# Performance work log

Hardware: AMD Instinct MI355X
Metric: run time of the kernel (lower is better)

The kernel has to match this reference:

```python
import jax, jax.numpy as jnp
import numpy as np

# dims
B, T, HORIZON, N = 32, 12, 12, 512
IN, OUT, H, P = 1, 1, 64, 32
S, ML, MG, DE = 12, 64, 32, 10  # S_local == S_global


def setup_inputs() -> dict:
    key = jax.random.key(0)
    ks = jax.random.split(key, 12)
    f = lambda k, shp: jax.random.normal(k, shp, dtype=jnp.float32)
    return {
        "source": f(ks[0], (B, T, N, IN)),
        "local_mem": f(ks[1], (ML, S, P)) * 0.1,
        "global_mem": f(ks[2], (MG, S, P)) * 0.1,
        "Wq": f(ks[3], (H, P)) / np.sqrt(H),
        "bq": jnp.zeros((P,), jnp.float32),
        "node_emb": f(ks[4], (N, DE)) * 0.1,
        "weight_pool": f(ks[5], (DE, 2 * P, H)) / np.sqrt(2 * P),
        "Wz": f(ks[6], (IN + H, H)) / np.sqrt(IN + H), "bz": jnp.zeros((H,), jnp.float32),
        "Wr": f(ks[7], (IN + H, H)) / np.sqrt(IN + H), "br": jnp.zeros((H,), jnp.float32),
        "Wc": f(ks[8], (IN + H, H)) / np.sqrt(IN + H), "bc": jnp.zeros((H,), jnp.float32),
        "Wo": f(ks[9], (H, OUT)) / np.sqrt(H), "bo": jnp.zeros((OUT,), jnp.float32),
    }


def _forward(source, local_mem, global_mem, Wq, bq, node_emb, weight_pool,
             Wz, bz, Wr, br, Wc, bc, Wo, bo):
    b, t, n, _ = source.shape
    hdim = Wz.shape[1]
    s = local_mem.shape[1]
    # node-specific hypernetwork weights: [N, 2P, H]
    nsw = jnp.einsum('nd,dfh->nfh', node_emb, weight_pool)
    lmean = local_mem.mean(axis=1)   # [ML, P]
    gmean = global_mem.mean(axis=1)  # [MG, P]

    def dcn(buffer):  # buffer: [B, N, S, H]
        q = jnp.einsum('bnsh,hp->bnsp', buffer, Wq) + bq          # [B,N,S,P]
        a_l = jax.nn.softmax(jnp.einsum('bnsp,msp->bnm', q, local_mem), axis=-1)
        a_g = jax.nn.softmax(jnp.einsum('bnsp,msp->bnm', q, global_mem), axis=-1)
        # context mean over S == attn @ mean-over-S memory
        lc = a_l @ lmean                                           # [B,N,P]
        gc = a_g @ gmean                                           # [B,N,P]
        fused = jnp.concatenate([lc, gc], axis=-1)                 # [B,N,2P]
        return jnp.einsum('bnf,nfh->bnh', fused, nsw)              # [B,N,H]

    def cell(x_t, h_prev, buffer):
        ctx = dcn(buffer)
        comb = jnp.concatenate([x_t, h_prev], axis=-1)
        z = jax.nn.sigmoid(comb @ Wz + bz)
        r = jax.nn.sigmoid(comb @ Wr + br)
        comb2 = jnp.concatenate([x_t, r * h_prev], axis=-1)
        hc = jnp.tanh(comb2 @ Wc + bc + ctx)
        return (1.0 - z) * h_prev + z * hc

    h0 = jnp.zeros((b, n, hdim), source.dtype)
    buf0 = jnp.zeros((b, n, s, hdim), source.dtype)

    def enc_step(carry, x_t):
        h, buf = carry
        h = cell(x_t, h, buf)
        buf = jax.lax.stop_gradient(
            jnp.concatenate([buf[:, :, 1:], h[:, :, None]], axis=2))
        return (h, buf), None

    (h, buf), _ = jax.lax.scan(enc_step, (h0, buf0), jnp.moveaxis(source, 1, 0))

    def dec_step(carry, _):
        h, buf, x = carry
        h = cell(x, h, buf)
        buf = jax.lax.stop_gradient(
            jnp.concatenate([buf[:, :, 1:], h[:, :, None]], axis=2))
        y = h @ Wo + bo
        return (h, buf, y), y

    _, ys = jax.lax.scan(dec_step, (h, buf, source[:, -1]), None, length=HORIZON)
    return jnp.moveaxis(ys, 0, 1)  # [B, horizon, N, OUT]


def reference(source, local_mem, global_mem, Wq, bq, node_emb, weight_pool,
              Wz, bz, Wr, br, Wc, bc, Wo, bo):
    return _forward(source, local_mem, global_mem, Wq, bq, node_emb, weight_pool,
                    Wz, bz, Wr, br, Wc, bc, Wo, bo)
```

## Files before the change

### kernel.cpp

```cpp
#include <hip/hip_runtime.h>


typedef short short8 __attribute__((ext_vector_type(8)));
typedef float f32x4 __attribute__((ext_vector_type(4)));

#define DEV static __device__ __forceinline__

DEV unsigned short f2bf(float f) {
  union { float f; unsigned u; } v; v.f = f;
  unsigned r = v.u + 0x7FFFu + ((v.u >> 16) & 1u);
  return (unsigned short)(r >> 16);
}
DEV float bf2f(unsigned short b) {
  union { unsigned u; float f; } v; v.u = ((unsigned)b) << 16;
  return v.f;
}
DEV unsigned cvtpk(float a, float b) {
  unsigned r;
  asm("v_cvt_pk_bf16_f32 %0, %1, %2" : "=v"(r) : "v"(a), "v"(b));
  return r;
}
DEV float rcpf(float x) { return __builtin_amdgcn_rcpf(x); }

#define WG_OFF  36864
#define WQ_OFF  61440
#define LM_OFF  63488
#define GM_OFF  65536
#define WS_TOT  66560

#define L_W     0
#define L_WQ    49152
#define L_LM    53248
#define L_SCR   59392
#define SCR_STRIDE 21504
#define SMEM_BYTES 145408

#define R_AL 0
#define R_AG 2048
#define R_FU 3072
#define R_HH 5120
#define R_HL 7168
#define R_RH 9216
#define R_RL 11264
#define R_NSW 13312
#define R_QQ 0

#define MFMA16(a, b, c) __builtin_amdgcn_mfma_f32_16x16x32_bf16((a), (b), (c), 0, 0, 0)

DEV int scat_off(int col, int g) {
  int kp = col & 31;
  return ((col >> 5) << 10) + ((kp >> 3) << 8) + (g << 6) + ((kp & 7) << 1);
}
DEV void scat4(char* p, f32x4 v) {
  unsigned p0 = cvtpk(v[0], v[1]), p1 = cvtpk(v[2], v[3]);
  *(unsigned short*)(p)      = (unsigned short)p0;
  *(unsigned short*)(p + 16) = (unsigned short)(p0 >> 16);
  *(unsigned short*)(p + 32) = (unsigned short)p1;
  *(unsigned short*)(p + 48) = (unsigned short)(p1 >> 16);
}
DEV void scat4_hilo(char* ph, char* pl, f32x4 v) {
  unsigned p0 = cvtpk(v[0], v[1]), p1 = cvtpk(v[2], v[3]);
  float h0 = __uint_as_float(p0 << 16), h1 = __uint_as_float(p0 & 0xFFFF0000u);
  float h2 = __uint_as_float(p1 << 16), h3 = __uint_as_float(p1 & 0xFFFF0000u);
  unsigned q0 = cvtpk(v[0] - h0, v[1] - h1), q1 = cvtpk(v[2] - h2, v[3] - h3);
  *(unsigned short*)(ph)      = (unsigned short)p0;
  *(unsigned short*)(ph + 16) = (unsigned short)(p0 >> 16);
  *(unsigned short*)(ph + 32) = (unsigned short)p1;
  *(unsigned short*)(ph + 48) = (unsigned short)(p1 >> 16);
  *(unsigned short*)(pl)      = (unsigned short)q0;
  *(unsigned short*)(pl + 16) = (unsigned short)(q0 >> 16);
  *(unsigned short*)(pl + 32) = (unsigned short)q1;
  *(unsigned short*)(pl + 48) = (unsigned short)(q1 >> 16);
}

__global__ __launch_bounds__(256, 1) void dyna_prep(
    const float* __restrict__ lmem, const float* __restrict__ gmem,
    const float* __restrict__ Wq, const float* __restrict__ Wz,
    const float* __restrict__ Wr, const float* __restrict__ Wc,
    unsigned short* __restrict__ ws)
{
  int i = blockIdx.x * 256 + threadIdx.x;
  if (i >= WS_TOT) return;

  if (i < WG_OFF) {
    int f = i >> 9, r = i & 511, lane = r >> 3, j = r & 7;
    int g = lane >> 4, u = lane & 15;
    int s = f / 6, nt = f % 6;
    int m = nt * 16 + u, p = g * 8 + j;
    float v = (m < 64) ? lmem[(m * 12 + s) * 32 + p]
                       : gmem[((m - 64) * 12 + s) * 32 + p];
    ws[i] = f2bf(v);
  } else if (i < WQ_OFF) {
    int t = i - WG_OFF;
    int f = t >> 9, r = t & 511, lane = r >> 3, j = r & 7;
    int g = lane >> 4, u = lane & 15;
    int hl = f & 1, kc = (f >> 1) & 1, nt = (f >> 2) & 3, gate = f >> 4;
    int k = kc * 32 + g * 8 + j, col = nt * 16 + u;
    const float* W = (gate == 0) ? Wz : (gate == 1) ? Wr : Wc;
    float w = W[(1 + k) * 64 + col];
    if (hl) { float hi = bf2f(f2bf(w)); ws[i] = f2bf(w - hi); }
    else ws[i] = f2bf(w);
  } else if (i < LM_OFF) {
    int t = i - WQ_OFF;
    int f = t >> 9, r = t & 511, lane = r >> 3, j = r & 7;
    int g = lane >> 4, u = lane & 15;
    int kc = f & 1, nt = f >> 1;
    int k = kc * 32 + g * 8 + j, col = nt * 16 + u;
    ws[i] = f2bf(Wq[k * 32 + col]);
  } else if (i < GM_OFF) {
    int t = i - LM_OFF;
    int f = t >> 9, r = t & 511, lane = r >> 3, j = r & 7;
    int g = lane >> 4, u = lane & 15;
    int kc = f >> 1, nt = f & 1;
    int k = kc * 32 + g * 8 + j, p = nt * 16 + u;
    float s = 0.f;
    for (int ss = 0; ss < 12; ++ss) s += lmem[(k * 12 + ss) * 32 + p];
    ws[i] = f2bf(s * (1.0f / 12.0f));
  } else {
    int t = i - GM_OFF;
    int f = t >> 9, r = t & 511, lane = r >> 3, j = r & 7;
    int g = lane >> 4, u = lane & 15;
    int nt = f;
    int k = g * 8 + j, p = nt * 16 + u;
    float s = 0.f;
    for (int ss = 0; ss < 12; ++ss) s += gmem[(k * 12 + ss) * 32 + p];
    ws[i] = f2bf(s * (1.0f / 12.0f));
  }
}

__global__ __launch_bounds__(256, 1) void dyna_main(
    const float* __restrict__ src, const float* __restrict__ emb,
    const float* __restrict__ pool, const float* __restrict__ bq,
    const float* __restrict__ Wz, const float* __restrict__ bz,
    const float* __restrict__ Wr, const float* __restrict__ br,
    const float* __restrict__ Wc, const float* __restrict__ bc,
    const float* __restrict__ Wo, const float* __restrict__ bo,
    const unsigned short* __restrict__ ws, float* __restrict__ out)
{
  extern __shared__ char smem[];
  const int tid = threadIdx.x;
  const int lane = tid & 63, wid = tid >> 6;
  const int g = lane >> 4, u = lane & 15;
  const int n = blockIdx.x * 2 + (wid >> 1);
  const int hb = wid & 1;

  {
    const short8* s8 = (const short8*)ws;
    short8* d8 = (short8*)smem;
    for (int i = tid; i < 3712; i += 256) d8[i] = s8[4608 + i];
  }

  short8 marr[72];
  #pragma unroll
  for (int f = 0; f < 72; ++f)
    marr[f] = *(const short8*)(ws + (f << 9) + lane * 8);

  char* SCR = smem + L_SCR + wid * SCR_STRIDE;

  #pragma unroll
  for (int kc = 0; kc < 2; ++kc)
    #pragma unroll
    for (int nt = 0; nt < 4; ++nt) {
      short8 v;
      #pragma unroll
      for (int j = 0; j < 8; ++j) {
        int k = kc * 32 + g * 8 + j, col = nt * 16 + u;
        float s = 0.f;
        #pragma unroll
        for (int d = 0; d < 10; ++d)
          s += emb[n * 10 + d] * pool[(d * 64 + k) * 64 + col];
        v[j] = (short)f2bf(s);
      }
      *(short8*)(SCR + R_NSW + ((kc * 4 + nt) << 10) + (lane << 4)) = v;
    }

  float w0z[4], w0r[4], w0c[4], bzv[4], brv[4], bcv[4], wov[4], bqv[2];
  #pragma unroll
  for (int nt = 0; nt < 4; ++nt) {
    int col = nt * 16 + u;
    w0z[nt] = Wz[col]; w0r[nt] = Wr[col]; w0c[nt] = Wc[col];
    bzv[nt] = bz[col]; brv[nt] = br[col]; bcv[nt] = bc[col];
    wov[nt] = Wo[col];
  }
  bqv[0] = bq[u]; bqv[1] = bq[16 + u];
  const float bov = bo[0];

  short8 qh[12];
  {
    short8 qi;
    #pragma unroll
    for (int j = 0; j < 8; ++j) qi[j] = (short)f2bf(bq[g * 8 + j]);
    #pragma unroll
    for (int s = 0; s < 12; ++s) qh[s] = qi;
  }
  f32x4 hreg[4];
  #pragma unroll
  for (int nt = 0; nt < 4; ++nt) hreg[nt] = (f32x4){0.f, 0.f, 0.f, 0.f};
  float xreg[4] = {0.f, 0.f, 0.f, 0.f};

  #pragma unroll
  for (int nt = 0; nt < 4; ++nt) {
    int so = scat_off(nt * 16 + u, g);
    scat4_hilo(SCR + R_HH + so, SCR + R_HL + so, hreg[nt]);
  }

  __syncthreads();

  for (int t = 0; t < 24; ++t) {
    if (t <= 12) {
      int tt = t < 12 ? t : 11;
      #pragma unroll
      for (int reg = 0; reg < 4; ++reg) {
        int b = hb * 16 + g * 4 + reg;
        xreg[reg] = src[(b * 12 + tt) * 512 + n];
      }
    }

    short8 hhi0 = *(const short8*)(SCR + R_HH + (lane << 4));
    short8 hhi1 = *(const short8*)(SCR + R_HH + 1024 + (lane << 4));
    short8 hlo0 = *(const short8*)(SCR + R_HL + (lane << 4));
    short8 hlo1 = *(const short8*)(SCR + R_HL + 1024 + (lane << 4));

    f32x4 sacc[6];
    #pragma unroll
    for (int nt = 0; nt < 6; ++nt) sacc[nt] = (f32x4){0.f, 0.f, 0.f, 0.f};
    __builtin_amdgcn_s_setprio(1);
    #pragma unroll
    for (int s = 0; s < 12; ++s) {
      #pragma unroll
      for (int nt = 0; nt < 6; ++nt)
        sacc[nt] = MFMA16(qh[s], marr[s * 6 + nt], sacc[nt]);
    }
    __builtin_amdgcn_s_setprio(0);

    #pragma unroll
    for (int nt = 0; nt < 6; ++nt)
      #pragma unroll
      for (int reg = 0; reg < 4; ++reg)
        sacc[nt][reg] = __expf(sacc[nt][reg]);
    float invl[4], invg[4];
    #pragma unroll
    for (int reg = 0; reg < 4; ++reg) {
      float sl = (sacc[0][reg] + sacc[1][reg]) + (sacc[2][reg] + sacc[3][reg]);
      sl += __shfl_xor(sl, 1); sl += __shfl_xor(sl, 2);
      sl += __shfl_xor(sl, 4); sl += __shfl_xor(sl, 8);
      invl[reg] = rcpf(sl);
      float sg = sacc[4][reg] + sacc[5][reg];
      sg += __shfl_xor(sg, 1); sg += __shfl_xor(sg, 2);
      sg += __shfl_xor(sg, 4); sg += __shfl_xor(sg, 8);
      invg[reg] = rcpf(sg);
    }

    #pragma unroll
    for (int nt = 0; nt < 4; ++nt)
      scat4(SCR + R_AL + scat_off(nt * 16 + u, g), sacc[nt]);
    #pragma unroll
    for (int nt = 0; nt < 2; ++nt)
      scat4(SCR + R_AG + scat_off(nt * 16 + u, g), sacc[4 + nt]);

    f32x4 zacc[4], racc[4];
    #pragma unroll
    for (int nt = 0; nt < 4; ++nt) {
      zacc[nt] = (f32x4){0.f, 0.f, 0.f, 0.f};
      racc[nt] = (f32x4){0.f, 0.f, 0.f, 0.f};
    }
    #pragma unroll
    for (int kc = 0; kc < 2; ++kc) {
      short8 hh = kc ? hhi1 : hhi0;
      short8 hl = kc ? hlo1 : hlo0;
      #pragma unroll
      for (int nt = 0; nt < 4; ++nt) {
        short8 wzh = *(const short8*)(smem + L_W + ((((0 + nt) * 2 + kc) * 2 + 0) << 10) + (lane << 4));
        short8 wzl = *(const short8*)(smem + L_W + ((((0 + nt) * 2 + kc) * 2 + 1) << 10) + (lane << 4));
        zacc[nt] = MFMA16(hh, wzh, zacc[nt]);
        zacc[nt] = MFMA16(hl, wzh, zacc[nt]);
        zacc[nt] = MFMA16(hh, wzl, zacc[nt]);
        short8 wrh = *(const short8*)(smem + L_W + ((((4 + nt) * 2 + kc) * 2 + 0) << 10) + (lane << 4));
        short8 wrl = *(const short8*)(smem + L_W + ((((4 + nt) * 2 + kc) * 2 + 1) << 10) + (lane << 4));
        racc[nt] = MFMA16(hh, wrh, racc[nt]);
        racc[nt] = MFMA16(hl, wrh, racc[nt]);
        racc[nt] = MFMA16(hh, wrl, racc[nt]);
      }
    }

    #pragma unroll
    for (int nt = 0; nt < 4; ++nt)
      #pragma unroll
      for (int reg = 0; reg < 4; ++reg) {
        float zv = zacc[nt][reg] + xreg[reg] * w0z[nt] + bzv[nt];
        zacc[nt][reg] = rcpf(1.0f + __expf(-zv));
        float rv = racc[nt][reg] + xreg[reg] * w0r[nt] + brv[nt];
        racc[nt][reg] = rcpf(1.0f + __expf(-rv));
      }

    #pragma unroll
    for (int nt = 0; nt < 4; ++nt) {
      int so = scat_off(nt * 16 + u, g);
      f32x4 rh;
      #pragma unroll
      for (int reg = 0; reg < 4; ++reg) rh[reg] = racc[nt][reg] * hreg[nt][reg];
      scat4_hilo(SCR + R_RH + so, SCR + R_RL + so, rh);
    }

    short8 alf0 = *(const short8*)(SCR + R_AL + (lane << 4));
    short8 alf1 = *(const short8*)(SCR + R_AL + 1024 + (lane << 4));
    short8 agf  = *(const short8*)(SCR + R_AG + (lane << 4));
    f32x4 lacc[2], gacc[2];
    #pragma unroll
    for (int nt = 0; nt < 2; ++nt) {
      lacc[nt] = (f32x4){0.f, 0.f, 0.f, 0.f};
      gacc[nt] = (f32x4){0.f, 0.f, 0.f, 0.f};
      short8 lm0 = *(const short8*)(smem + L_LM + ((0 * 2 + nt) << 10) + (lane << 4));
      short8 lm1 = *(const short8*)(smem + L_LM + ((1 * 2 + nt) << 10) + (lane << 4));
      short8 gm  = *(const short8*)(smem + L_LM + 4096 + (nt << 10) + (lane << 4));
      lacc[nt] = MFMA16(alf0, lm0, lacc[nt]);
      lacc[nt] = MFMA16(alf1, lm1, lacc[nt]);
      gacc[nt] = MFMA16(agf, gm, gacc[nt]);
    }

    short8 rhh0 = *(const short8*)(SCR + R_RH + (lane << 4));
    short8 rhh1 = *(const short8*)(SCR + R_RH + 1024 + (lane << 4));
    short8 rhl0 = *(const short8*)(SCR + R_RL + (lane << 4));
    short8 rhl1 = *(const short8*)(SCR + R_RL + 1024 + (lane << 4));
    f32x4 hacc[4];
    #pragma unroll
    for (int nt = 0; nt < 4; ++nt) hacc[nt] = (f32x4){0.f, 0.f, 0.f, 0.f};
    #pragma unroll
    for (int kc = 0; kc < 2; ++kc) {
      short8 hh = kc ? rhh1 : rhh0;
      short8 hl = kc ? rhl1 : rhl0;
      #pragma unroll
      for (int nt = 0; nt < 4; ++nt) {
        short8 wch = *(const short8*)(smem + L_W + ((((8 + nt) * 2 + kc) * 2 + 0) << 10) + (lane << 4));
        short8 wcl = *(const short8*)(smem + L_W + ((((8 + nt) * 2 + kc) * 2 + 1) << 10) + (lane << 4));
        hacc[nt] = MFMA16(hh, wch, hacc[nt]);
        hacc[nt] = MFMA16(hl, wch, hacc[nt]);
        hacc[nt] = MFMA16(hh, wcl, hacc[nt]);
      }
    }

    #pragma unroll
    for (int nt = 0; nt < 2; ++nt) {
      f32x4 lv, gv;
      #pragma unroll
      for (int reg = 0; reg < 4; ++reg) {
        lv[reg] = lacc[nt][reg] * invl[reg];
        gv[reg] = gacc[nt][reg] * invg[reg];
      }
      scat4(SCR + R_FU + scat_off(nt * 16 + u, g), lv);
      scat4(SCR + R_FU + scat_off(32 + nt * 16 + u, g), gv);
    }
    short8 fuf0 = *(const short8*)(SCR + R_FU + (lane << 4));
    short8 fuf1 = *(const short8*)(SCR + R_FU + 1024 + (lane << 4));

    f32x4 cacc[4];
    #pragma unroll
    for (int nt = 0; nt < 4; ++nt) {
      short8 nf0 = *(const short8*)(SCR + R_NSW + ((0 * 4 + nt) << 10) + (lane << 4));
      short8 nf1 = *(const short8*)(SCR + R_NSW + ((1 * 4 + nt) << 10) + (lane << 4));
      cacc[nt] = (f32x4){0.f, 0.f, 0.f, 0.f};
      cacc[nt] = MFMA16(fuf0, nf0, cacc[nt]);
      cacc[nt] = MFMA16(fuf1, nf1, cacc[nt]);
    }

    #pragma unroll
    for (int nt = 0; nt < 4; ++nt)
      #pragma unroll
      for (int reg = 0; reg < 4; ++reg) {
        float pv = hacc[nt][reg] + cacc[nt][reg] + xreg[reg] * w0c[nt] + bcv[nt];
        float tdenom = rcpf(1.0f + __expf(2.0f * pv));
        float hc = 1.0f - 2.0f * tdenom;
        float zv = zacc[nt][reg];
        hreg[nt][reg] = (1.0f - zv) * hreg[nt][reg] + zv * hc;
      }

    #pragma unroll
    for (int nt = 0; nt < 4; ++nt) {
      int so = scat_off(nt * 16 + u, g);
      scat4_hilo(SCR + R_HH + so, SCR + R_HL + so, hreg[nt]);
    }
    short8 nh0 = *(const short8*)(SCR + R_HH + (lane << 4));
    short8 nh1 = *(const short8*)(SCR + R_HH + 1024 + (lane << 4));

    f32x4 qacc[2];
    #pragma unroll
    for (int nt = 0; nt < 2; ++nt) {
      short8 wq0 = *(const short8*)(smem + L_WQ + ((nt * 2 + 0) << 10) + (lane << 4));
      short8 wq1 = *(const short8*)(smem + L_WQ + ((nt * 2 + 1) << 10) + (lane << 4));
      qacc[nt] = (f32x4){0.f, 0.f, 0.f, 0.f};
      qacc[nt] = MFMA16(nh0, wq0, qacc[nt]);
      qacc[nt] = MFMA16(nh1, wq1, qacc[nt]);
      #pragma unroll
      for (int reg = 0; reg < 4; ++reg) qacc[nt][reg] += bqv[nt];
    }
    #pragma unroll
    for (int nt = 0; nt < 2; ++nt)
      scat4(SCR + R_QQ + scat_off(nt * 16 + u, g), qacc[nt]);
    short8 qnf = *(const short8*)(SCR + R_QQ + (lane << 4));
    #pragma unroll
    for (int s = 0; s < 11; ++s) qh[s] = qh[s + 1];
    qh[11] = qnf;

    if (t >= 12) {
      #pragma unroll
      for (int reg = 0; reg < 4; ++reg) {
        float yp = hreg[0][reg] * wov[0] + hreg[1][reg] * wov[1] +
                   hreg[2][reg] * wov[2] + hreg[3][reg] * wov[3];
        yp += __shfl_xor(yp, 1); yp += __shfl_xor(yp, 2);
        yp += __shfl_xor(yp, 4); yp += __shfl_xor(yp, 8);
        float yv = yp + bov;
        xreg[reg] = yv;
        if (u == 0) {
          int b = hb * 16 + g * 4 + reg;
          out[(b * 12 + (t - 12)) * 512 + n] = yv;
        }
      }
    }
  }
}

extern "C" void kernel_launch(void* const* d_in, const int* in_sizes, int n_in,
                              void* d_out, int out_size, void* d_ws, size_t ws_size,
                              hipStream_t stream) {
  const float* src  = (const float*)d_in[0];
  const float* lmem = (const float*)d_in[1];
  const float* gmem = (const float*)d_in[2];
  const float* Wq   = (const float*)d_in[3];
  const float* bq   = (const float*)d_in[4];
  const float* emb  = (const float*)d_in[5];
  const float* pool = (const float*)d_in[6];
  const float* Wz   = (const float*)d_in[7];
  const float* bz   = (const float*)d_in[8];
  const float* Wr   = (const float*)d_in[9];
  const float* br   = (const float*)d_in[10];
  const float* Wc   = (const float*)d_in[11];
  const float* bc   = (const float*)d_in[12];
  const float* Wo   = (const float*)d_in[13];
  const float* bo   = (const float*)d_in[14];
  float* out = (float*)d_out;
  unsigned short* ws = (unsigned short*)d_ws;

  dyna_prep<<<260, 256, 0, stream>>>(lmem, gmem, Wq, Wz, Wr, Wc, ws);

  (void)hipFuncSetAttribute((const void*)dyna_main,
                            hipFuncAttributeMaxDynamicSharedMemorySize,
                            SMEM_BYTES);
  dyna_main<<<256, 256, SMEM_BYTES, stream>>>(src, emb, pool, bq, Wz, bz, Wr, br,
                                              Wc, bc, Wo, bo, ws, out);
}
```

Measured before the change: 211.9 us.

## Precompute next-step attention scores and offload row reductions to MFMA

The attention-score MFMA chain is restructured so that the 11 of 12 query-history terms still valid after the history shift are accumulated mid-step for the next timestep. This leaves only one MFMA per tile on the critical path at the start of each step, and the rest can overlap with the gate GEMMs. Softmax denominators now come from MFMA against an all-ones bf16 matrix instead of cross-lane shuffles. The decoder output projection uses split-bf16 MFMA in place of a shuffle reduction. The costs are extra live accumulator registers, and denominators built from bf16-rounded exponentials.

```diff
diff --git a/kernel.cpp b/kernel.cpp
--- a/kernel.cpp
+++ b/kernel.cpp
@@ -143,6 +143,7 @@
   const int g = lane >> 4, u = lane & 15;
   const int n = blockIdx.x * 2 + (wid >> 1);
   const int hb = wid & 1;
+  const f32x4 ZERO4 = {0.f, 0.f, 0.f, 0.f};
 
   {
     const short8* s8 = (const short8*)ws;
@@ -174,13 +175,25 @@
       *(short8*)(SCR + R_NSW + ((kc * 4 + nt) << 10) + (lane << 4)) = v;
     }
 
-  float w0z[4], w0r[4], w0c[4], bzv[4], brv[4], bcv[4], wov[4], bqv[2];
+  short8 ones, woh[2], wol[2];
+  #pragma unroll
+  for (int j = 0; j < 8; ++j) ones[j] = (short)0x3F80;
+  #pragma unroll
+  for (int kc = 0; kc < 2; ++kc)
+    #pragma unroll
+    for (int j = 0; j < 8; ++j) {
+      float w = Wo[kc * 32 + g * 8 + j];
+      unsigned short hi = f2bf(w);
+      woh[kc][j] = (short)hi;
+      wol[kc][j] = (short)f2bf(w - bf2f(hi));
+    }
+
+  float w0z[4], w0r[4], w0c[4], bzv[4], brv[4], bcv[4], bqv[2];
   #pragma unroll
   for (int nt = 0; nt < 4; ++nt) {
     int col = nt * 16 + u;
     w0z[nt] = Wz[col]; w0r[nt] = Wr[col]; w0c[nt] = Wc[col];
     bzv[nt] = bz[col]; brv[nt] = br[col]; bcv[nt] = bc[col];
-    wov[nt] = Wo[col];
   }
   bqv[0] = bq[u]; bqv[1] = bq[16 + u];
   const float bov = bo[0];
@@ -195,8 +208,17 @@
   }
   f32x4 hreg[4];
   #pragma unroll
-  for (int nt = 0; nt < 4; ++nt) hreg[nt] = (f32x4){0.f, 0.f, 0.f, 0.f};
+  for (int nt = 0; nt < 4; ++nt) hreg[nt] = ZERO4;
   float xreg[4] = {0.f, 0.f, 0.f, 0.f};
+
+  f32x4 sacc_next[6];
+  #pragma unroll
+  for (int nt = 0; nt < 6; ++nt) sacc_next[nt] = ZERO4;
+  #pragma unroll
+  for (int s = 0; s <= 10; ++s)
+    #pragma unroll
+    for (int nt = 0; nt < 6; ++nt)
+      sacc_next[nt] = MFMA16(qh[s], marr[s * 6 + nt], sacc_next[nt]);
 
   #pragma unroll
   for (int nt = 0; nt < 4; ++nt) {
@@ -223,34 +245,14 @@
 
     f32x4 sacc[6];
     #pragma unroll
-    for (int nt = 0; nt < 6; ++nt) sacc[nt] = (f32x4){0.f, 0.f, 0.f, 0.f};
-    __builtin_amdgcn_s_setprio(1);
-    #pragma unroll
-    for (int s = 0; s < 12; ++s) {
-      #pragma unroll
-      for (int nt = 0; nt < 6; ++nt)
-        sacc[nt] = MFMA16(qh[s], marr[s * 6 + nt], sacc[nt]);
-    }
-    __builtin_amdgcn_s_setprio(0);
+    for (int nt = 0; nt < 6; ++nt)
+      sacc[nt] = MFMA16(qh[11], marr[66 + nt], sacc_next[nt]);
 
     #pragma unroll
     for (int nt = 0; nt < 6; ++nt)
       #pragma unroll
       for (int reg = 0; reg < 4; ++reg)
         sacc[nt][reg] = __expf(sacc[nt][reg]);
-    float invl[4], invg[4];
-    #pragma unroll
-    for (int reg = 0; reg < 4; ++reg) {
-      float sl = (sacc[0][reg] + sacc[1][reg]) + (sacc[2][reg] + sacc[3][reg]);
-      sl += __shfl_xor(sl, 1); sl += __shfl_xor(sl, 2);
-      sl += __shfl_xor(sl, 4); sl += __shfl_xor(sl, 8);
-      invl[reg] = rcpf(sl);
-      float sg = sacc[4][reg] + sacc[5][reg];
-      sg += __shfl_xor(sg, 1); sg += __shfl_xor(sg, 2);
-      sg += __shfl_xor(sg, 4); sg += __shfl_xor(sg, 8);
-      invg[reg] = rcpf(sg);
-    }
-
     #pragma unroll
     for (int nt = 0; nt < 4; ++nt)
       scat4(SCR + R_AL + scat_off(nt * 16 + u, g), sacc[nt]);
@@ -258,11 +260,19 @@
     for (int nt = 0; nt < 2; ++nt)
       scat4(SCR + R_AG + scat_off(nt * 16 + u, g), sacc[4 + nt]);
 
+    #pragma unroll
+    for (int nt = 0; nt < 6; ++nt) sacc_next[nt] = ZERO4;
+    #pragma unroll
+    for (int s = 1; s <= 11; ++s)
+      #pragma unroll
+      for (int nt = 0; nt < 6; ++nt)
+        sacc_next[nt] = MFMA16(qh[s], marr[(s - 1) * 6 + nt], sacc_next[nt]);
+
     f32x4 zacc[4], racc[4];
     #pragma unroll
     for (int nt = 0; nt < 4; ++nt) {
-      zacc[nt] = (f32x4){0.f, 0.f, 0.f, 0.f};
-      racc[nt] = (f32x4){0.f, 0.f, 0.f, 0.f};
+      zacc[nt] = ZERO4;
+      racc[nt] = ZERO4;
     }
     #pragma unroll
     for (int kc = 0; kc < 2; ++kc) {
@@ -305,11 +315,16 @@
     short8 alf0 = *(const short8*)(SCR + R_AL + (lane << 4));
     short8 alf1 = *(const short8*)(SCR + R_AL + 1024 + (lane << 4));
     short8 agf  = *(const short8*)(SCR + R_AG + (lane << 4));
+    f32x4 lsum = ZERO4;
+    lsum = MFMA16(alf0, ones, lsum);
+    lsum = MFMA16(alf1, ones, lsum);
+    f32x4 gsum = ZERO4;
+    gsum = MFMA16(agf, ones, gsum);
     f32x4 lacc[2], gacc[2];
     #pragma unroll
     for (int nt = 0; nt < 2; ++nt) {
-      lacc[nt] = (f32x4){0.f, 0.f, 0.f, 0.f};
-      gacc[nt] = (f32x4){0.f, 0.f, 0.f, 0.f};
+      lacc[nt] = ZERO4;
+      gacc[nt] = ZERO4;
       short8 lm0 = *(const short8*)(smem + L_LM + ((0 * 2 + nt) << 10) + (lane << 4));
       short8 lm1 = *(const short8*)(smem + L_LM + ((1 * 2 + nt) << 10) + (lane << 4));
       short8 gm  = *(const short8*)(smem + L_LM + 4096 + (nt << 10) + (lane << 4));
@@ -324,7 +339,7 @@
     short8 rhl1 = *(const short8*)(SCR + R_RL + 1024 + (lane << 4));
     f32x4 hacc[4];
     #pragma unroll
-    for (int nt = 0; nt < 4; ++nt) hacc[nt] = (f32x4){0.f, 0.f, 0.f, 0.f};
+    for (int nt = 0; nt < 4; ++nt) hacc[nt] = ZERO4;
     #pragma unroll
     for (int kc = 0; kc < 2; ++kc) {
       short8 hh = kc ? rhh1 : rhh0;
@@ -339,6 +354,12 @@
       }
     }
 
+    float invl[4], invg[4];
+    #pragma unroll
+    for (int reg = 0; reg < 4; ++reg) {
+      invl[reg] = rcpf(lsum[reg]);
+      invg[reg] = rcpf(gsum[reg]);
+    }
     #pragma unroll
     for (int nt = 0; nt < 2; ++nt) {
       f32x4 lv, gv;
@@ -358,7 +379,7 @@
     for (int nt = 0; nt < 4; ++nt) {
       short8 nf0 = *(const short8*)(SCR + R_NSW + ((0 * 4 + nt) << 10) + (lane << 4));
       short8 nf1 = *(const short8*)(SCR + R_NSW + ((1 * 4 + nt) << 10) + (lane << 4));
-      cacc[nt] = (f32x4){0.f, 0.f, 0.f, 0.f};
+      cacc[nt] = ZERO4;
       cacc[nt] = MFMA16(fuf0, nf0, cacc[nt]);
       cacc[nt] = MFMA16(fuf1, nf1, cacc[nt]);
     }
@@ -387,7 +408,7 @@
     for (int nt = 0; nt < 2; ++nt) {
       short8 wq0 = *(const short8*)(smem + L_WQ + ((nt * 2 + 0) << 10) + (lane << 4));
       short8 wq1 = *(const short8*)(smem + L_WQ + ((nt * 2 + 1) << 10) + (lane << 4));
-      qacc[nt] = (f32x4){0.f, 0.f, 0.f, 0.f};
+      qacc[nt] = ZERO4;
       qacc[nt] = MFMA16(nh0, wq0, qacc[nt]);
       qacc[nt] = MFMA16(nh1, wq1, qacc[nt]);
       #pragma unroll
@@ -402,13 +423,18 @@
     qh[11] = qnf;
 
     if (t >= 12) {
+      short8 nhl0 = *(const short8*)(SCR + R_HL + (lane << 4));
+      short8 nhl1 = *(const short8*)(SCR + R_HL + 1024 + (lane << 4));
+      f32x4 yacc = ZERO4;
+      yacc = MFMA16(nh0, woh[0], yacc);
+      yacc = MFMA16(nhl0, woh[0], yacc);
+      yacc = MFMA16(nh0, wol[0], yacc);
+      yacc = MFMA16(nh1, woh[1], yacc);
+      yacc = MFMA16(nhl1, woh[1], yacc);
+      yacc = MFMA16(nh1, wol[1], yacc);
       #pragma unroll
       for (int reg = 0; reg < 4; ++reg) {
-        float yp = hreg[0][reg] * wov[0] + hreg[1][reg] * wov[1] +
-                   hreg[2][reg] * wov[2] + hreg[3][reg] * wov[3];
-        yp += __shfl_xor(yp, 1); yp += __shfl_xor(yp, 2);
-        yp += __shfl_xor(yp, 4); yp += __shfl_xor(yp, 8);
-        float yv = yp + bov;
+        float yv = yacc[reg] + bov;
         xreg[reg] = yv;
         if (u == 0) {
           int b = hb * 16 + g * 4 + reg;
```

New measurement: 218.2 us. 1.03x slower.
